# Performance work log

Hardware: AMD Instinct MI355X
Metric: run time of the kernel (lower is better)

Reference implementation:

```python
import jax, jax.numpy as jnp
import numpy as np

WINDOW = 60
DEPTH = 3
HIDDEN = 256
LN_EPS = 1e-5


def _lyndon_indices(d):
    # Lyndon words over alphabet {0..d-1}, lengths 2 and 3, lexicographic order
    # (signatory mode='words' extracts expanded-logsig coefficients at Lyndon words).
    i2 = np.array([(i, j) for i in range(d) for j in range(d) if (i, j) < (j, i)], dtype=np.int32)
    i3 = np.array([(i, j, k) for i in range(d) for j in range(d) for k in range(d)
                   if (i, j, k) < (j, k, i) and (i, j, k) < (k, i, j)], dtype=np.int32)
    return i2, i3


def _logsig_features(x):
    # x: [b, s, c] -> logsignature of time-augmented sliding windows: [b*s, sig_channels]
    b, s, c = x.shape
    d = c + 1
    # replicate-padded sliding windows via clipped gather (matches F.pad replicate + unfold)
    pos = jnp.clip(jnp.arange(s)[:, None] + jnp.arange(WINDOW)[None, :] - (WINDOW - 1), 0, s - 1)
    windows = x[:, pos, :]                                   # [b, s, W, c]
    t = jnp.linspace(0.0, 1.0, WINDOW, dtype=x.dtype)        # time augmentation channel
    t_b = jnp.broadcast_to(t[None, None, :, None], (b, s, WINDOW, 1))
    aug = jnp.concatenate([t_b, windows], axis=-1).reshape(b * s, WINDOW, d)
    N = b * s
    # basepoint=True: prepend zero point -> increments include the first point itself
    inc = jnp.diff(aug, axis=1, prepend=jnp.zeros((N, 1, d), aug.dtype))  # [N, W, d]
    inc_t = jnp.transpose(inc, (1, 0, 2))                    # [W, N, d]

    def chen_step(carry, v):
        S1, S2, S3 = carry
        vv = jnp.einsum('ni,nj->nij', v, v)
        vvv = jnp.einsum('nij,nk->nijk', vv, v)
        nS3 = S3 + jnp.einsum('nij,nk->nijk', S2, v) \
                 + 0.5 * jnp.einsum('ni,njk->nijk', S1, vv) + vvv / 6.0
        nS2 = S2 + jnp.einsum('ni,nj->nij', S1, v) + 0.5 * vv
        nS1 = S1 + v
        return (nS1, nS2, nS3), None

    init = (jnp.zeros((N, d), x.dtype), jnp.zeros((N, d, d), x.dtype), jnp.zeros((N, d, d, d), x.dtype))
    (S1, S2, S3), _ = jax.lax.scan(chen_step, init, inc_t)
    # log in truncated tensor algebra: log(1+x) = x - x^2/2 + x^3/3
    L1 = S1
    L2 = S2 - 0.5 * jnp.einsum('ni,nj->nij', S1, S1)
    L3 = (S3 - 0.5 * (jnp.einsum('ni,njk->nijk', S1, S2) + jnp.einsum('nij,nk->nijk', S2, S1))
          + jnp.einsum('ni,nj,nk->nijk', S1, S1, S1) / 3.0)
    i2, i3 = _lyndon_indices(d)
    f2 = L2[:, i2[:, 0], i2[:, 1]]
    f3 = L3[:, i3[:, 0], i3[:, 1], i3[:, 2]]
    return jnp.concatenate([L1, f2, f3], axis=-1)            # [N, sig_channels]


def setup_inputs() -> dict:
    key = jax.random.key(0)
    ks = jax.random.split(key, 5)
    b, s, c = 8, 2048, 8
    d = c + 1
    sig_channels = d + (d * d - d) // 2 + (d ** 3 - d) // 3  # 285 for d=9
    h2 = 2 * HIDDEN
    x = jax.random.normal(ks[0], (b, s, c), dtype=jnp.float32)
    w1 = jax.random.normal(ks[1], (sig_channels, h2), dtype=jnp.float32) / np.sqrt(sig_channels)
    b1 = jnp.zeros((h2,), jnp.float32)
    ln_g = jnp.ones((h2,), jnp.float32)
    ln_b = jnp.zeros((h2,), jnp.float32)
    w2 = jax.random.normal(ks[2], (h2, HIDDEN), dtype=jnp.float32) / np.sqrt(h2)
    b2 = jnp.zeros((HIDDEN,), jnp.float32)
    return {"x": x, "w1": w1, "b1": b1, "ln_g": ln_g, "ln_b": ln_b, "w2": w2, "b2": b2}


def reference(x, w1, b1, ln_g, ln_b, w2, b2):
    b, s, _ = x.shape
    feats = _logsig_features(x)                              # [b*s, sig_channels]
    h = jax.nn.gelu(feats @ w1 + b1, approximate=False)      # torch default GELU (erf)
    mu = jnp.mean(h, axis=-1, keepdims=True)
    var = jnp.var(h, axis=-1, keepdims=True)
    h = (h - mu) / jnp.sqrt(var + LN_EPS) * ln_g + ln_b      # LayerNorm; Dropout is eval no-op
    out = h @ w2 + b2
    return out.reshape(b, s, -1)
```

## Files before the change

kernel.cpp:

```cpp
#include <hip/hip_runtime.h>
#include <hip/hip_bf16.h>
#include <cstdint>
#include <cstddef>

typedef short short8 __attribute__((ext_vector_type(8)));
typedef float f32x4 __attribute__((ext_vector_type(4)));

#define NS    2048
#define KPAD  288
#define H2    512
#define HID   256
#define WPB   21
#define SBLK  98

__device__ __forceinline__ void gl2lds16(const void* g, void* l) {
    __builtin_amdgcn_global_load_lds(
        (const __attribute__((address_space(1))) void*)g,
        (__attribute__((address_space(3))) void*)l, 16, 0, 0);
}

__device__ __forceinline__ float geluf(float x) {
    return 0.5f * x * (1.0f + erff(x * 0.70710678118654752f));
}

__device__ __forceinline__ f32x4 shfl4(f32x4 v, int d) {
    f32x4 r;
    r[0] = __shfl_xor(v[0], d); r[1] = __shfl_xor(v[1], d);
    r[2] = __shfl_xor(v[2], d); r[3] = __shfl_xor(v[3], d);
    return r;
}

struct Tbl3 { short col[729]; };
static constexpr Tbl3 make_tbl3() {
    Tbl3 t{};
    for (int x = 0; x < 729; ++x) t.col[x] = -1;
    int r = 0;
    for (int i = 0; i < 9; ++i)
        for (int j = 0; j < 9; ++j)
            for (int k = 0; k < 9; ++k) {
                bool lt1 = (i < j) || (i == j && (j < k || (j == k && k < i)));
                bool lt2 = (i < k) || (i == k && (j < i || (j == i && k < j)));
                if (lt1 && lt2) { t.col[(i*9+j)*9+k] = (short)(45 + r); ++r; }
            }
    return t;
}
static constexpr Tbl3 TBL3 = make_tbl3();

#define SIG_STEP(RA,RB,RC) { \
    const float hh = 0.5f * S1i + vi * (1.0f / 6.0f); \
    { const float ra = S2ra + hh * v##RA; \
      S3a0 += ra*v0; S3a1 += ra*v1; S3a2 += ra*v2; S3a3 += ra*v3; S3a4 += ra*v4; \
      S3a5 += ra*v5; S3a6 += ra*v6; S3a7 += ra*v7; S3a8 += ra*v8; } \
    { const float rb = S2rb + hh * v##RB; \
      S3b0 += rb*v0; S3b1 += rb*v1; S3b2 += rb*v2; S3b3 += rb*v3; S3b4 += rb*v4; \
      S3b5 += rb*v5; S3b6 += rb*v6; S3b7 += rb*v7; S3b8 += rb*v8; } \
    { const float rc = S2rc + hh * v##RC; \
      S3c0 += rc*v0; S3c1 += rc*v1; S3c2 += rc*v2; S3c3 += rc*v3; S3c4 += rc*v4; \
      S3c5 += rc*v5; S3c6 += rc*v6; S3c7 += rc*v7; S3c8 += rc*v8; } \
    const float aa = S1i + 0.5f * vi; \
    S2ra += aa * v##RA; S2rb += aa * v##RB; S2rc += aa * v##RC; \
    S1i += vi; }

#define SIG_MAIN(RA,RB,RC) { \
     \
    const float* xr = &X[(g0 - lo) * 8]; \
    const float4 e0p = *(const float4*)xr; \
    const float4 e1p = *(const float4*)(xr + 4); \
    const float rabs = xr[ioff]; \
    { const float v0 = 0.f; \
      const float v1 = e0p.x, v2 = e0p.y, v3 = e0p.z, v4 = e0p.w; \
      const float v5 = e1p.x, v6 = e1p.y, v7 = e1p.z, v8 = e1p.w; \
      const float vi = (ci == 0) ? 0.f : rabs; \
      SIG_STEP(RA,RB,RC) } \
     \
    int gn = sm59 + 1; gn = (gn > 0) ? gn : 0; \
    const float* dp = &D[(gn - lo) * 8]; \
    float4 d0 = *(const float4*)dp; \
    float4 d1 = *(const float4*)(dp + 4); \
    float rn = dp[ioff]; \
    _Pragma("unroll 1") \
    for (int j = 1; j < 60; ++j) { \
      const float4 e0 = d0; const float4 e1 = d1; const float rs = rn; \
      int g2 = sm59 + j + 1; g2 = (g2 > 0) ? g2 : 0; \
      const float* dn = &D[(g2 - lo) * 8]; \
      d0 = *(const float4*)dn; d1 = *(const float4*)(dn + 4); rn = dn[ioff]; \
      const float v0 = DT; \
      const float v1 = e0.x, v2 = e0.y, v3 = e0.z, v4 = e0.w; \
      const float v5 = e1.x, v6 = e1.y, v7 = e1.z, v8 = e1.w; \
      const float vi = (ci == 0) ? DT : rs; \
      SIG_STEP(RA,RB,RC) \
    } }

#define SIG_ST(RA,RB,RC) \
    if (act) { \
        if ((RA) == 0) S1buf[widx * 9 + ci] = S1i; \
        float* sb = &S2buf[widx * 81 + ci * 9]; \
        sb[RA] = S2ra; sb[RB] = S2rb; sb[RC] = S2rc; \
    }

#define SIG_E2(SL,J2) if (ci < (J2)) { \
    const float val2 = S2r##SL - 0.5f * S1i * s1v##J2; \
    const int col2 = 9 + ci*8 - (ci*(ci-1))/2 + ((J2) - ci - 1); \
    frow[col2] = __float2bfloat16(val2); }

#define SIG_E3(SL,R,K) { const int col3 = TBL3.col[tb + (R)*9 + (K)]; \
    if (col3 >= 0) { \
        const float val3 = S3##SL##K \
            - 0.5f * (S1i * S2w[(R)*9+(K)] + S2r##SL * s1v##K) \
            + S1i * s1v##R * s1v##K * (1.0f/3.0f); \
        frow[col3] = __float2bfloat16(val3); } }

#define SIG_E3R(SL,R) SIG_E3(SL,R,0) SIG_E3(SL,R,1) SIG_E3(SL,R,2) SIG_E3(SL,R,3) \
    SIG_E3(SL,R,4) SIG_E3(SL,R,5) SIG_E3(SL,R,6) SIG_E3(SL,R,7) SIG_E3(SL,R,8)

#define SIG_EMIT(RA,RB,RC) \
    if (act) { \
        if ((RA) == 0) { \
            frow[ci] = __float2bfloat16(S1i); \
            if (ci == 0) { \
                const __hip_bfloat16 z16 = __float2bfloat16(0.0f); \
                frow[285] = z16; frow[286] = z16; frow[287] = z16; \
            } \
        } \
        SIG_E2(a,RA) SIG_E2(b,RB) SIG_E2(c,RC) \
        SIG_E3R(a,RA) SIG_E3R(b,RB) SIG_E3R(c,RC) \
    }

__global__ __launch_bounds__(576) __attribute__((amdgpu_waves_per_eu(1, 6)))
void sig_kernel(const float* __restrict__ x, __hip_bfloat16* __restrict__ feats) {
    __shared__ __align__(16) float X[82 * 8];
    __shared__ __align__(16) float D[82 * 8];
    __shared__ float S2buf[WPB * 81];
    __shared__ float S1buf[WPB * 9];

    const int blk = blockIdx.x;
    const int b   = blk / SBLK;
    const int s0  = (blk % SBLK) * WPB;
    const int lo  = (s0 - 59 > 0) ? (s0 - 59) : 0;
    const int hi  = (s0 + WPB - 1 < NS - 1) ? (s0 + WPB - 1) : (NS - 1);
    const int nrow = hi - lo + 1;
    const int tid = threadIdx.x;

    {
        const float4* src = (const float4*)(x + ((size_t)b * NS + lo) * 8);
        float4* dst = (float4*)X;
        const int n4 = nrow * 2;
        for (int t = tid; t < n4; t += 576) dst[t] = src[t];
    }
    __syncthreads();
    {
        const float4* X4 = (const float4*)X;
        float4* D4 = (float4*)D;
        for (int t = tid; t < 164; t += 576) {
            const int r = t >> 1;
            float4 dv = {0.f, 0.f, 0.f, 0.f};
            if (r > 0 && r < nrow) {
                const float4 a = X4[t], bb = X4[t - 2];
                dv.x = a.x - bb.x; dv.y = a.y - bb.y; dv.z = a.z - bb.z; dv.w = a.w - bb.w;
            }
            D4[t] = dv;
        }
    }
    __syncthreads();

    const int t3    = tid / 192;
    const int lt    = tid - t3 * 192;
    const int widx0 = lt / 9;
    const int ci    = lt - widx0 * 9;
    const int s_raw = s0 + widx0;
    const bool act  = (lt < 189) && (s_raw < NS);
    const int widx  = (widx0 < 20) ? widx0 : 20;
    int s = s0 + widx; if (s > NS - 1) s = NS - 1;

    float S3a0=0.f,S3a1=0.f,S3a2=0.f,S3a3=0.f,S3a4=0.f,S3a5=0.f,S3a6=0.f,S3a7=0.f,S3a8=0.f;
    float S3b0=0.f,S3b1=0.f,S3b2=0.f,S3b3=0.f,S3b4=0.f,S3b5=0.f,S3b6=0.f,S3b7=0.f,S3b8=0.f;
    float S3c0=0.f,S3c1=0.f,S3c2=0.f,S3c3=0.f,S3c4=0.f,S3c5=0.f,S3c6=0.f,S3c7=0.f,S3c8=0.f;
    float S2ra=0.f, S2rb=0.f, S2rc=0.f;
    float S1i = 0.f;
    const int ioff = (ci > 0) ? (ci - 1) : 0;
    const int sm59 = s - 59;
    const int g0   = (sm59 > 0) ? sm59 : 0;
    const float DT = 1.0f / 59.0f;

    if (t3 == 0)      { SIG_MAIN(0,1,2) }
    else if (t3 == 1) { SIG_MAIN(3,4,5) }
    else              { SIG_MAIN(6,7,8) }

    if (t3 == 0)      { SIG_ST(0,1,2) }
    else if (t3 == 1) { SIG_ST(3,4,5) }
    else              { SIG_ST(6,7,8) }
    __syncthreads();

    const float* s1p = &S1buf[widx * 9];
    const float s1v0=s1p[0], s1v1=s1p[1], s1v2=s1p[2], s1v3=s1p[3], s1v4=s1p[4];
    const float s1v5=s1p[5], s1v6=s1p[6], s1v7=s1p[7], s1v8=s1p[8];
    const float* S2w = &S2buf[widx * 81];
    const int tb = ci * 81;
    __hip_bfloat16* frow = feats + (size_t)(b * NS + s) * KPAD;

    if (t3 == 0)      { SIG_EMIT(0,1,2) }
    else if (t3 == 1) { SIG_EMIT(3,4,5) }
    else              { SIG_EMIT(6,7,8) }
}

__global__ void convert_w1(const float* __restrict__ w1, __hip_bfloat16* __restrict__ w1T) {
    const int n = blockIdx.x;
    const int k = threadIdx.x;
    const float v = (k < 285) ? w1[(size_t)k * H2 + n] : 0.0f;
    w1T[(size_t)n * KPAD + k] = __float2bfloat16(v);
}
__global__ void convert_w2(const float* __restrict__ w2, __hip_bfloat16* __restrict__ w2T) {
    const int n = blockIdx.x;
    const int k = threadIdx.x;
    w2T[(size_t)n * H2 + k] = __float2bfloat16(w2[(size_t)k * HID + n]);
}

#define G1_DECLACC(m) f32x4 acc##m##0 = {0.f,0.f,0.f,0.f}, acc##m##1 = {0.f,0.f,0.f,0.f}, \
                            acc##m##2 = {0.f,0.f,0.f,0.f}, acc##m##3 = {0.f,0.f,0.f,0.f};
#define G1_MFMA(m) { const short8 afr = *(const short8*)(ldsA + ((m)*16 + l16)*32 + quad*8); \
    acc##m##0 = __builtin_amdgcn_mfma_f32_16x16x32_bf16(afr, bfrag0, acc##m##0, 0,0,0); \
    acc##m##1 = __builtin_amdgcn_mfma_f32_16x16x32_bf16(afr, bfrag1, acc##m##1, 0,0,0); \
    acc##m##2 = __builtin_amdgcn_mfma_f32_16x16x32_bf16(afr, bfrag2, acc##m##2, 0,0,0); \
    acc##m##3 = __builtin_amdgcn_mfma_f32_16x16x32_bf16(afr, bfrag3, acc##m##3, 0,0,0); }
#define G1_GELU1(m,n) { \
    acc##m##n[0]=geluf(acc##m##n[0]+bias##n); acc##m##n[1]=geluf(acc##m##n[1]+bias##n); \
    acc##m##n[2]=geluf(acc##m##n[2]+bias##n); acc##m##n[3]=geluf(acc##m##n[3]+bias##n); }
#define G1_GELUR(m) G1_GELU1(m,0) G1_GELU1(m,1) G1_GELU1(m,2) G1_GELU1(m,3)
#define G1_LNS(m) f32x4 psum##m = acc##m##0 + acc##m##1 + acc##m##2 + acc##m##3; \
    f32x4 psq##m = acc##m##0*acc##m##0 + acc##m##1*acc##m##1 + acc##m##2*acc##m##2 + acc##m##3*acc##m##3;
#define G1_STP(m) { const int rrp = (m)*16 + quad*4; \
    lnpart[wave][rrp+0][0]=psum##m[0]; lnpart[wave][rrp+0][1]=psq##m[0]; \
    lnpart[wave][rrp+1][0]=psum##m[1]; lnpart[wave][rrp+1][1]=psq##m[1]; \
    lnpart[wave][rrp+2][0]=psum##m[2]; lnpart[wave][rrp+2][1]=psq##m[2]; \
    lnpart[wave][rrp+3][0]=psum##m[3]; lnpart[wave][rrp+3][1]=psq##m[3]; }
#define G1_LDST(m) f32x4 mu##m; f32x4 rstd##m; { const int rrl = (m)*16 + quad*4; \
    mu##m[0]=lnstat[rrl+0][0]; mu##m[1]=lnstat[rrl+1][0]; mu##m[2]=lnstat[rrl+2][0]; mu##m[3]=lnstat[rrl+3][0]; \
    rstd##m[0]=lnstat[rrl+0][1]; rstd##m[1]=lnstat[rrl+1][1]; rstd##m[2]=lnstat[rrl+2][1]; rstd##m[3]=lnstat[rrl+3][1]; }
#define G1_OUT(m,n) { const int colo = wave*64 + (n)*16 + l16; \
    f32x4 hv = (acc##m##n - mu##m) * rstd##m * gv##n + bv##n; \
    const int rro = (m)*16 + quad*4; \
    hbuf[(size_t)(m0+rro+0)*H2 + colo] = __float2bfloat16(hv[0]); \
    hbuf[(size_t)(m0+rro+1)*H2 + colo] = __float2bfloat16(hv[1]); \
    hbuf[(size_t)(m0+rro+2)*H2 + colo] = __float2bfloat16(hv[2]); \
    hbuf[(size_t)(m0+rro+3)*H2 + colo] = __float2bfloat16(hv[3]); }
#define G1_OUTR(m) G1_OUT(m,0) G1_OUT(m,1) G1_OUT(m,2) G1_OUT(m,3)

__global__ __launch_bounds__(512) __attribute__((amdgpu_waves_per_eu(1, 4)))
void gemm1_kernel(
        const __hip_bfloat16* __restrict__ feats,
        const __hip_bfloat16* __restrict__ w1T,
        const float* __restrict__ b1,
        const float* __restrict__ lng,
        const float* __restrict__ lnb,
        __hip_bfloat16* __restrict__ hbuf) {
    __shared__ __align__(16) __hip_bfloat16 ldsA[32 * 32];
    __shared__ __align__(16) __hip_bfloat16 ldsB[512 * 32];
    __shared__ float lnpart[8][32][2];
    __shared__ float lnstat[32][2];

    const int tid  = threadIdx.x;
    const int wave = tid >> 6;
    const int lane = tid & 63;
    const int quad = lane >> 4;
    const int l16  = lane & 15;
    const int m0   = blockIdx.x * 32;

    G1_DECLACC(0) G1_DECLACC(1)

#pragma unroll 1
    for (int kt = 0; kt < 9; ++kt) {
        const int K0 = kt * 32;
        if (tid < 128) {
            const int m = tid >> 2, kc = tid & 3;
            gl2lds16(feats + (size_t)(m0 + m) * KPAD + K0 + kc * 8,
                     (char*)ldsA + (tid & ~63) * 16);
        }
#pragma unroll
        for (int q = 0; q < 4; ++q) {
            const int chunk = q * 512 + tid;
            const int n = chunk >> 2, kc = chunk & 3;
            gl2lds16(w1T + (size_t)n * KPAD + K0 + kc * 8,
                     (char*)ldsB + (chunk & ~63) * 16);
        }
        __syncthreads();
        const __hip_bfloat16* bbase = ldsB + (wave * 64 + l16) * 32 + quad * 8;
        const short8 bfrag0 = *(const short8*)(bbase);
        const short8 bfrag1 = *(const short8*)(bbase + 16 * 32);
        const short8 bfrag2 = *(const short8*)(bbase + 32 * 32);
        const short8 bfrag3 = *(const short8*)(bbase + 48 * 32);
        G1_MFMA(0) G1_MFMA(1)
        __syncthreads();
    }

    const float bias0 = b1[wave*64 +  0 + l16];
    const float bias1 = b1[wave*64 + 16 + l16];
    const float bias2 = b1[wave*64 + 32 + l16];
    const float bias3 = b1[wave*64 + 48 + l16];
    G1_GELUR(0) G1_GELUR(1)

    G1_LNS(0) G1_LNS(1)
#pragma unroll
    for (int d = 1; d < 16; d <<= 1) {
        psum0 += shfl4(psum0, d); psq0 += shfl4(psq0, d);
        psum1 += shfl4(psum1, d); psq1 += shfl4(psq1, d);
    }
    if (l16 == 0) { G1_STP(0) G1_STP(1) }
    __syncthreads();
    if (tid < 32) {
        float su = 0.f, sq = 0.f;
#pragma unroll
        for (int w = 0; w < 8; ++w) { su += lnpart[w][tid][0]; sq += lnpart[w][tid][1]; }
        const float mu  = su * (1.0f / 512.0f);
        const float var = sq * (1.0f / 512.0f) - mu * mu;
        lnstat[tid][0] = mu;
        lnstat[tid][1] = rsqrtf(var + 1e-5f);
    }
    __syncthreads();
    const float gv0 = lng[wave*64 +  0 + l16], bv0 = lnb[wave*64 +  0 + l16];
    const float gv1 = lng[wave*64 + 16 + l16], bv1 = lnb[wave*64 + 16 + l16];
    const float gv2 = lng[wave*64 + 32 + l16], bv2 = lnb[wave*64 + 32 + l16];
    const float gv3 = lng[wave*64 + 48 + l16], bv3 = lnb[wave*64 + 48 + l16];
    G1_LDST(0) G1_LDST(1)
    G1_OUTR(0) G1_OUTR(1)
}

#define G2_DECL(m) f32x4 bcc##m##0 = {0.f,0.f,0.f,0.f}, bcc##m##1 = {0.f,0.f,0.f,0.f};
#define G2_MFMA(m) { const short8 afr = *(const short8*)(ldsA + ((m)*16 + l16)*32 + quad*8); \
    bcc##m##0 = __builtin_amdgcn_mfma_f32_16x16x32_bf16(afr, bfr0, bcc##m##0, 0,0,0); \
    bcc##m##1 = __builtin_amdgcn_mfma_f32_16x16x32_bf16(afr, bfr1, bcc##m##1, 0,0,0); }
#define G2_OUT(m) { const int rro = (m)*16 + quad*4; \
    out[(size_t)(m0+rro+0)*HID + c0i] = bcc##m##0[0] + bb0; \
    out[(size_t)(m0+rro+1)*HID + c0i] = bcc##m##0[1] + bb0; \
    out[(size_t)(m0+rro+2)*HID + c0i] = bcc##m##0[2] + bb0; \
    out[(size_t)(m0+rro+3)*HID + c0i] = bcc##m##0[3] + bb0; \
    out[(size_t)(m0+rro+0)*HID + c1i] = bcc##m##1[0] + bb1; \
    out[(size_t)(m0+rro+1)*HID + c1i] = bcc##m##1[1] + bb1; \
    out[(size_t)(m0+rro+2)*HID + c1i] = bcc##m##1[2] + bb1; \
    out[(size_t)(m0+rro+3)*HID + c1i] = bcc##m##1[3] + bb1; }

__global__ __launch_bounds__(512) __attribute__((amdgpu_waves_per_eu(1, 4)))
void gemm2_kernel(
        const __hip_bfloat16* __restrict__ hbuf,
        const __hip_bfloat16* __restrict__ w2T,
        const float* __restrict__ b2,
        float* __restrict__ out) {
    __shared__ __align__(16) __hip_bfloat16 ldsA[32 * 32];
    __shared__ __align__(16) __hip_bfloat16 ldsB[256 * 32];
    const int tid  = threadIdx.x;
    const int wave = tid >> 6;
    const int lane = tid & 63;
    const int quad = lane >> 4;
    const int l16  = lane & 15;
    const int m0   = blockIdx.x * 32;

    G2_DECL(0) G2_DECL(1)

#pragma unroll 1
    for (int kt = 0; kt < 16; ++kt) {
        const int K0 = kt * 32;
        if (tid < 128) {
            const int m = tid >> 2, kc = tid & 3;
            gl2lds16(hbuf + (size_t)(m0 + m) * H2 + K0 + kc * 8,
                     (char*)ldsA + (tid & ~63) * 16);
        }
#pragma unroll
        for (int q = 0; q < 2; ++q) {
            const int chunk = q * 512 + tid;
            const int n = chunk >> 2, kc = chunk & 3;
            gl2lds16(w2T + (size_t)n * H2 + K0 + kc * 8,
                     (char*)ldsB + (chunk & ~63) * 16);
        }
        __syncthreads();
        const __hip_bfloat16* bbase = ldsB + (wave * 32 + l16) * 32 + quad * 8;
        const short8 bfr0 = *(const short8*)(bbase);
        const short8 bfr1 = *(const short8*)(bbase + 16 * 32);
        G2_MFMA(0) G2_MFMA(1)
        __syncthreads();
    }
    const float bb0 = b2[wave*32 +  0 + l16];
    const float bb1 = b2[wave*32 + 16 + l16];
    const int c0i = wave*32 +  0 + l16;
    const int c1i = wave*32 + 16 + l16;
    G2_OUT(0) G2_OUT(1)
}

extern "C" void kernel_launch(void* const* d_in, const int* in_sizes, int n_in,
                              void* d_out, int out_size, void* d_ws, size_t ws_size,
                              hipStream_t stream) {
    const float* x   = (const float*)d_in[0];
    const float* w1  = (const float*)d_in[1];
    const float* b1  = (const float*)d_in[2];
    const float* lng = (const float*)d_in[3];
    const float* lnb = (const float*)d_in[4];
    const float* w2  = (const float*)d_in[5];
    const float* b2  = (const float*)d_in[6];
    float* out = (float*)d_out;

    char* ws = (char*)d_ws;
    __hip_bfloat16* feats = (__hip_bfloat16*)(ws);
    __hip_bfloat16* hbuf  = (__hip_bfloat16*)(ws + 9437184);
    __hip_bfloat16* w1T   = (__hip_bfloat16*)(ws + 9437184 + 16777216);
    __hip_bfloat16* w2T   = (__hip_bfloat16*)(ws + 9437184 + 16777216 + 294912);

    convert_w1<<<dim3(512), dim3(288), 0, stream>>>(w1, w1T);
    convert_w2<<<dim3(256), dim3(512), 0, stream>>>(w2, w2T);
    sig_kernel<<<dim3(8 * SBLK), dim3(576), 0, stream>>>(x, feats);
    gemm1_kernel<<<dim3(16384 / 32), dim3(512), 0, stream>>>(feats, w1T, b1, lng, lnb, hbuf);
    gemm2_kernel<<<dim3(16384 / 32), dim3(512), 0, stream>>>(hbuf, w2T, b2, out);
}
```

Baseline: 171.8 us.

## Retile GEMMs to 128x128, fold LayerNorm into GEMM2 epilogue, reshape sig kernel

Both GEMMs now use 128x128 tiles per 256-thread block instead of 32-row strips that reload the whole weight matrix for every block. LayerNorm is no longer applied in GEMM1: row sums and sums of squares are accumulated with atomics, and the gamma, beta and bias terms are folded into a pre-scaled W2 plus per-column vectors, so GEMM2 applies the normalization algebraically in its epilogue. The signature kernel moves to smaller blocks of 7 windows with a pre-padded increment buffer that removes per-step clamping, and uses packed float2 FMAs. In exchange the GELU output is stored un-normalized in bf16, the variance is computed as E[x^2]-mu^2, and an extra memset plus atomic traffic are added.

```diff
diff --git a/kernel.cpp b/kernel.cpp
--- a/kernel.cpp
+++ b/kernel.cpp
@@ -5,24 +5,25 @@
 
 typedef short short8 __attribute__((ext_vector_type(8)));
 typedef float f32x4 __attribute__((ext_vector_type(4)));
+typedef float f32x2 __attribute__((ext_vector_type(2)));
 
 #define NS    2048
 #define KPAD  288
 #define H2    512
 #define HID   256
-#define WPB   21
-#define SBLK  98
+#define WPB   7
+#define SBLK  293
+
+#define MFMA(a,b,c) __builtin_amdgcn_mfma_f32_16x16x32_bf16((a),(b),(c),0,0,0)
 
 __device__ __forceinline__ void gl2lds16(const void* g, void* l) {
     __builtin_amdgcn_global_load_lds(
         (const __attribute__((address_space(1))) void*)g,
         (__attribute__((address_space(3))) void*)l, 16, 0, 0);
 }
-
 __device__ __forceinline__ float geluf(float x) {
     return 0.5f * x * (1.0f + erff(x * 0.70710678118654752f));
 }
-
 __device__ __forceinline__ f32x4 shfl4(f32x4 v, int d) {
     f32x4 r;
     r[0] = __shfl_xor(v[0], d); r[1] = __shfl_xor(v[1], d);
@@ -46,49 +47,41 @@
 }
 static constexpr Tbl3 TBL3 = make_tbl3();
 
-#define SIG_STEP(RA,RB,RC) { \
-    const float hh = 0.5f * S1i + vi * (1.0f / 6.0f); \
-    { const float ra = S2ra + hh * v##RA; \
-      S3a0 += ra*v0; S3a1 += ra*v1; S3a2 += ra*v2; S3a3 += ra*v3; S3a4 += ra*v4; \
-      S3a5 += ra*v5; S3a6 += ra*v6; S3a7 += ra*v7; S3a8 += ra*v8; } \
-    { const float rb = S2rb + hh * v##RB; \
-      S3b0 += rb*v0; S3b1 += rb*v1; S3b2 += rb*v2; S3b3 += rb*v3; S3b4 += rb*v4; \
-      S3b5 += rb*v5; S3b6 += rb*v6; S3b7 += rb*v7; S3b8 += rb*v8; } \
-    { const float rc = S2rc + hh * v##RC; \
-      S3c0 += rc*v0; S3c1 += rc*v1; S3c2 += rc*v2; S3c3 += rc*v3; S3c4 += rc*v4; \
-      S3c5 += rc*v5; S3c6 += rc*v6; S3c7 += rc*v7; S3c8 += rc*v8; } \
+#define SIG_STEP(VA_,VB_,VC_) { \
+    const float hh = 0.5f * S1i + vi * (1.0f/6.0f); \
+    const float ra = S2ra + hh * (VA_); \
+    const float rb = S2rb + hh * (VB_); \
+    const float rc = S2rc + hh * (VC_); \
+    const f32x2 ra2 = {ra, ra}, rb2 = {rb, rb}, rc2 = {rc, rc}; \
+    S3sa += ra * v0; S3pa0 += ra2*vp0; S3pa1 += ra2*vp1; S3pa2 += ra2*vp2; S3pa3 += ra2*vp3; \
+    S3sb += rb * v0; S3pb0 += rb2*vp0; S3pb1 += rb2*vp1; S3pb2 += rb2*vp2; S3pb3 += rb2*vp3; \
+    S3sc += rc * v0; S3pc0 += rc2*vp0; S3pc1 += rc2*vp1; S3pc2 += rc2*vp2; S3pc3 += rc2*vp3; \
     const float aa = S1i + 0.5f * vi; \
-    S2ra += aa * v##RA; S2rb += aa * v##RB; S2rc += aa * v##RC; \
+    S2ra += aa * (VA_); S2rb += aa * (VB_); S2rc += aa * (VC_); \
     S1i += vi; }
 
-#define SIG_MAIN(RA,RB,RC) { \
-     \
-    const float* xr = &X[(g0 - lo) * 8]; \
-    const float4 e0p = *(const float4*)xr; \
-    const float4 e1p = *(const float4*)(xr + 4); \
-    const float rabs = xr[ioff]; \
-    { const float v0 = 0.f; \
-      const float v1 = e0p.x, v2 = e0p.y, v3 = e0p.z, v4 = e0p.w; \
-      const float v5 = e1p.x, v6 = e1p.y, v7 = e1p.z, v8 = e1p.w; \
-      const float vi = (ci == 0) ? 0.f : rabs; \
-      SIG_STEP(RA,RB,RC) } \
-     \
-    int gn = sm59 + 1; gn = (gn > 0) ? gn : 0; \
-    const float* dp = &D[(gn - lo) * 8]; \
-    float4 d0 = *(const float4*)dp; \
-    float4 d1 = *(const float4*)(dp + 4); \
-    float rn = dp[ioff]; \
-    _Pragma("unroll 1") \
+#define SIG_MAIN(VA_,VB_,VC_) { \
+    { const float* xr = &X[(g0 - lo) * 8]; \
+      const float4 e0 = *(const float4*)xr; \
+      const float4 e1 = *(const float4*)(xr + 4); \
+      const float rs = xr[ioff]; \
+      const float v0 = 0.0f; \
+      const f32x2 vp0 = {e0.x, e0.y}, vp1 = {e0.z, e0.w}, vp2 = {e1.x, e1.y}, vp3 = {e1.z, e1.w}; \
+      const float vi = (ci == 0) ? 0.0f : rs; \
+      SIG_STEP(VA_,VB_,VC_) } \
+    const float* pd = &PD[(sm59 + 1 - lo + 59) * 8]; \
+    float4 d0 = *(const float4*)pd; \
+    float4 d1 = *(const float4*)(pd + 4); \
+    float rn = pd[ioff]; \
+    _Pragma("unroll 2") \
     for (int j = 1; j < 60; ++j) { \
       const float4 e0 = d0; const float4 e1 = d1; const float rs = rn; \
-      int g2 = sm59 + j + 1; g2 = (g2 > 0) ? g2 : 0; \
-      const float* dn = &D[(g2 - lo) * 8]; \
-      d0 = *(const float4*)dn; d1 = *(const float4*)(dn + 4); rn = dn[ioff]; \
+      pd += 8; \
+      d0 = *(const float4*)pd; d1 = *(const float4*)(pd + 4); rn = pd[ioff]; \
       const float v0 = DT; \
-      const float v1 = e0.x, v2 = e0.y, v3 = e0.z, v4 = e0.w; \
-      const float v5 = e1.x, v6 = e1.y, v7 = e1.z, v8 = e1.w; \
+      const f32x2 vp0 = {e0.x, e0.y}, vp1 = {e0.z, e0.w}, vp2 = {e1.x, e1.y}, vp3 = {e1.z, e1.w}; \
       const float vi = (ci == 0) ? DT : rs; \
-      SIG_STEP(RA,RB,RC) \
+      SIG_STEP(VA_,VB_,VC_) \
     } }
 
 #define SIG_ST(RA,RB,RC) \
@@ -98,6 +91,16 @@
         sb[RA] = S2ra; sb[RB] = S2rb; sb[RC] = S2rc; \
     }
 
+#define S3EL0(SL) S3s##SL
+#define S3EL1(SL) S3p##SL##0[0]
+#define S3EL2(SL) S3p##SL##0[1]
+#define S3EL3(SL) S3p##SL##1[0]
+#define S3EL4(SL) S3p##SL##1[1]
+#define S3EL5(SL) S3p##SL##2[0]
+#define S3EL6(SL) S3p##SL##2[1]
+#define S3EL7(SL) S3p##SL##3[0]
+#define S3EL8(SL) S3p##SL##3[1]
+
 #define SIG_E2(SL,J2) if (ci < (J2)) { \
     const float val2 = S2r##SL - 0.5f * S1i * s1v##J2; \
     const int col2 = 9 + ci*8 - (ci*(ci-1))/2 + ((J2) - ci - 1); \
@@ -105,7 +108,7 @@
 
 #define SIG_E3(SL,R,K) { const int col3 = TBL3.col[tb + (R)*9 + (K)]; \
     if (col3 >= 0) { \
-        const float val3 = S3##SL##K \
+        const float val3 = S3EL##K(SL) \
             - 0.5f * (S1i * S2w[(R)*9+(K)] + S2r##SL * s1v##K) \
             + S1i * s1v##R * s1v##K * (1.0f/3.0f); \
         frow[col3] = __float2bfloat16(val3); } }
@@ -126,10 +129,10 @@
         SIG_E3R(a,RA) SIG_E3R(b,RB) SIG_E3R(c,RC) \
     }
 
-__global__ __launch_bounds__(576) __attribute__((amdgpu_waves_per_eu(1, 6)))
+__global__ __launch_bounds__(192) __attribute__((amdgpu_waves_per_eu(1, 6)))
 void sig_kernel(const float* __restrict__ x, __hip_bfloat16* __restrict__ feats) {
-    __shared__ __align__(16) float X[82 * 8];
-    __shared__ __align__(16) float D[82 * 8];
+    __shared__ __align__(16) float X[66 * 8];
+    __shared__ __align__(16) float PD[126 * 8];
     __shared__ float S2buf[WPB * 81];
     __shared__ float S1buf[WPB * 9];
 
@@ -143,38 +146,39 @@
 
     {
         const float4* src = (const float4*)(x + ((size_t)b * NS + lo) * 8);
-        float4* dst = (float4*)X;
+        float4* X4 = (float4*)X;
         const int n4 = nrow * 2;
-        for (int t = tid; t < n4; t += 576) dst[t] = src[t];
+        for (int t = tid; t < n4; t += 192) X4[t] = src[t];
     }
     __syncthreads();
     {
         const float4* X4 = (const float4*)X;
-        float4* D4 = (float4*)D;
-        for (int t = tid; t < 164; t += 576) {
-            const int r = t >> 1;
+        float4* PD4 = (float4*)PD;
+        for (int t = tid; t < 252; t += 192) {
+            const int p = t >> 1;
+            const int r = p - 59;
             float4 dv = {0.f, 0.f, 0.f, 0.f};
             if (r > 0 && r < nrow) {
-                const float4 a = X4[t], bb = X4[t - 2];
+                const float4 a = X4[t - 118], bb = X4[t - 120];
                 dv.x = a.x - bb.x; dv.y = a.y - bb.y; dv.z = a.z - bb.z; dv.w = a.w - bb.w;
             }
-            D4[t] = dv;
+            PD4[t] = dv;
         }
     }
     __syncthreads();
 
-    const int t3    = tid / 192;
-    const int lt    = tid - t3 * 192;
+    const int t3    = tid >> 6;
+    const int lt    = tid & 63;
     const int widx0 = lt / 9;
     const int ci    = lt - widx0 * 9;
-    const int s_raw = s0 + widx0;
-    const bool act  = (lt < 189) && (s_raw < NS);
-    const int widx  = (widx0 < 20) ? widx0 : 20;
+    const bool act  = (lt < 63) && (s0 + widx0 < NS);
+    const int widx  = (widx0 < WPB - 1) ? widx0 : WPB - 1;
     int s = s0 + widx; if (s > NS - 1) s = NS - 1;
 
-    float S3a0=0.f,S3a1=0.f,S3a2=0.f,S3a3=0.f,S3a4=0.f,S3a5=0.f,S3a6=0.f,S3a7=0.f,S3a8=0.f;
-    float S3b0=0.f,S3b1=0.f,S3b2=0.f,S3b3=0.f,S3b4=0.f,S3b5=0.f,S3b6=0.f,S3b7=0.f,S3b8=0.f;
-    float S3c0=0.f,S3c1=0.f,S3c2=0.f,S3c3=0.f,S3c4=0.f,S3c5=0.f,S3c6=0.f,S3c7=0.f,S3c8=0.f;
+    float S3sa=0.f, S3sb=0.f, S3sc=0.f;
+    f32x2 S3pa0={0.f,0.f},S3pa1={0.f,0.f},S3pa2={0.f,0.f},S3pa3={0.f,0.f};
+    f32x2 S3pb0={0.f,0.f},S3pb1={0.f,0.f},S3pb2={0.f,0.f},S3pb3={0.f,0.f};
+    f32x2 S3pc0={0.f,0.f},S3pc1={0.f,0.f},S3pc2={0.f,0.f},S3pc3={0.f,0.f};
     float S2ra=0.f, S2rb=0.f, S2rc=0.f;
     float S1i = 0.f;
     const int ioff = (ci > 0) ? (ci - 1) : 0;
@@ -182,9 +186,9 @@
     const int g0   = (sm59 > 0) ? sm59 : 0;
     const float DT = 1.0f / 59.0f;
 
-    if (t3 == 0)      { SIG_MAIN(0,1,2) }
-    else if (t3 == 1) { SIG_MAIN(3,4,5) }
-    else              { SIG_MAIN(6,7,8) }
+    if (t3 == 0)      { SIG_MAIN(v0,   e0.x, e0.y) }
+    else if (t3 == 1) { SIG_MAIN(e0.z, e0.w, e1.x) }
+    else              { SIG_MAIN(e1.y, e1.z, e1.w) }
 
     if (t3 == 0)      { SIG_ST(0,1,2) }
     else if (t3 == 1) { SIG_ST(3,4,5) }
@@ -209,179 +213,149 @@
     const float v = (k < 285) ? w1[(size_t)k * H2 + n] : 0.0f;
     w1T[(size_t)n * KPAD + k] = __float2bfloat16(v);
 }
-__global__ void convert_w2(const float* __restrict__ w2, __hip_bfloat16* __restrict__ w2T) {
-    const int n = blockIdx.x;
-    const int k = threadIdx.x;
-    w2T[(size_t)n * H2 + k] = __float2bfloat16(w2[(size_t)k * HID + n]);
-}
-
-#define G1_DECLACC(m) f32x4 acc##m##0 = {0.f,0.f,0.f,0.f}, acc##m##1 = {0.f,0.f,0.f,0.f}, \
-                            acc##m##2 = {0.f,0.f,0.f,0.f}, acc##m##3 = {0.f,0.f,0.f,0.f};
-#define G1_MFMA(m) { const short8 afr = *(const short8*)(ldsA + ((m)*16 + l16)*32 + quad*8); \
-    acc##m##0 = __builtin_amdgcn_mfma_f32_16x16x32_bf16(afr, bfrag0, acc##m##0, 0,0,0); \
-    acc##m##1 = __builtin_amdgcn_mfma_f32_16x16x32_bf16(afr, bfrag1, acc##m##1, 0,0,0); \
-    acc##m##2 = __builtin_amdgcn_mfma_f32_16x16x32_bf16(afr, bfrag2, acc##m##2, 0,0,0); \
-    acc##m##3 = __builtin_amdgcn_mfma_f32_16x16x32_bf16(afr, bfrag3, acc##m##3, 0,0,0); }
-#define G1_GELU1(m,n) { \
-    acc##m##n[0]=geluf(acc##m##n[0]+bias##n); acc##m##n[1]=geluf(acc##m##n[1]+bias##n); \
-    acc##m##n[2]=geluf(acc##m##n[2]+bias##n); acc##m##n[3]=geluf(acc##m##n[3]+bias##n); }
-#define G1_GELUR(m) G1_GELU1(m,0) G1_GELU1(m,1) G1_GELU1(m,2) G1_GELU1(m,3)
-#define G1_LNS(m) f32x4 psum##m = acc##m##0 + acc##m##1 + acc##m##2 + acc##m##3; \
-    f32x4 psq##m = acc##m##0*acc##m##0 + acc##m##1*acc##m##1 + acc##m##2*acc##m##2 + acc##m##3*acc##m##3;
-#define G1_STP(m) { const int rrp = (m)*16 + quad*4; \
-    lnpart[wave][rrp+0][0]=psum##m[0]; lnpart[wave][rrp+0][1]=psq##m[0]; \
-    lnpart[wave][rrp+1][0]=psum##m[1]; lnpart[wave][rrp+1][1]=psq##m[1]; \
-    lnpart[wave][rrp+2][0]=psum##m[2]; lnpart[wave][rrp+2][1]=psq##m[2]; \
-    lnpart[wave][rrp+3][0]=psum##m[3]; lnpart[wave][rrp+3][1]=psq##m[3]; }
-#define G1_LDST(m) f32x4 mu##m; f32x4 rstd##m; { const int rrl = (m)*16 + quad*4; \
-    mu##m[0]=lnstat[rrl+0][0]; mu##m[1]=lnstat[rrl+1][0]; mu##m[2]=lnstat[rrl+2][0]; mu##m[3]=lnstat[rrl+3][0]; \
-    rstd##m[0]=lnstat[rrl+0][1]; rstd##m[1]=lnstat[rrl+1][1]; rstd##m[2]=lnstat[rrl+2][1]; rstd##m[3]=lnstat[rrl+3][1]; }
-#define G1_OUT(m,n) { const int colo = wave*64 + (n)*16 + l16; \
-    f32x4 hv = (acc##m##n - mu##m) * rstd##m * gv##n + bv##n; \
-    const int rro = (m)*16 + quad*4; \
-    hbuf[(size_t)(m0+rro+0)*H2 + colo] = __float2bfloat16(hv[0]); \
-    hbuf[(size_t)(m0+rro+1)*H2 + colo] = __float2bfloat16(hv[1]); \
-    hbuf[(size_t)(m0+rro+2)*H2 + colo] = __float2bfloat16(hv[2]); \
-    hbuf[(size_t)(m0+rro+3)*H2 + colo] = __float2bfloat16(hv[3]); }
-#define G1_OUTR(m) G1_OUT(m,0) G1_OUT(m,1) G1_OUT(m,2) G1_OUT(m,3)
-
-__global__ __launch_bounds__(512) __attribute__((amdgpu_waves_per_eu(1, 4)))
-void gemm1_kernel(
-        const __hip_bfloat16* __restrict__ feats,
-        const __hip_bfloat16* __restrict__ w1T,
-        const float* __restrict__ b1,
-        const float* __restrict__ lng,
-        const float* __restrict__ lnb,
-        __hip_bfloat16* __restrict__ hbuf) {
-    __shared__ __align__(16) __hip_bfloat16 ldsA[32 * 32];
-    __shared__ __align__(16) __hip_bfloat16 ldsB[512 * 32];
-    __shared__ float lnpart[8][32][2];
-    __shared__ float lnstat[32][2];
-
+__global__ void convert_w2g(const float* __restrict__ w2, const float* __restrict__ lng,
+                            const float* __restrict__ lnb, const float* __restrict__ b2,
+                            __hip_bfloat16* __restrict__ w2g, float* __restrict__ gw,
+                            float* __restrict__ cvec) {
+    const int n = blockIdx.x, k = threadIdx.x;
+    const float wv = w2[(size_t)k * HID + n];
+    const float a = lng[k] * wv;
+    const float c = lnb[k] * wv;
+    w2g[(size_t)n * H2 + k] = __float2bfloat16(a);
+    float ra = a, rc = c;
+#pragma unroll
+    for (int d = 1; d < 64; d <<= 1) { ra += __shfl_xor(ra, d); rc += __shfl_xor(rc, d); }
+    __shared__ float r1[8], r2[8];
+    const int wv_ = k >> 6, ln = k & 63;
+    if (ln == 0) { r1[wv_] = ra; r2[wv_] = rc; }
+    __syncthreads();
+    if (k == 0) {
+        float sa = 0.f, sc = 0.f;
+#pragma unroll
+        for (int i = 0; i < 8; ++i) { sa += r1[i]; sc += r2[i]; }
+        gw[n] = sa; cvec[n] = sc + b2[n];
+    }
+}
+
+#define GDECL \
+    f32x4 acc00={0,0,0,0},acc01={0,0,0,0},acc02={0,0,0,0},acc03={0,0,0,0}; \
+    f32x4 acc10={0,0,0,0},acc11={0,0,0,0},acc12={0,0,0,0},acc13={0,0,0,0}; \
+    f32x4 acc20={0,0,0,0},acc21={0,0,0,0},acc22={0,0,0,0},acc23={0,0,0,0}; \
+    f32x4 acc30={0,0,0,0},acc31={0,0,0,0},acc32={0,0,0,0},acc33={0,0,0,0};
+
+#define GMROW(mf) { const short8 av = *(const short8*)(abase + (mf)*512); \
+    acc##mf##0 = MFMA(av, b0v, acc##mf##0); acc##mf##1 = MFMA(av, b1v, acc##mf##1); \
+    acc##mf##2 = MFMA(av, b2v, acc##mf##2); acc##mf##3 = MFMA(av, b3v, acc##mf##3); }
+
+#define GEMM_KLOOP(APTR, BPTR, KD, KSTEPS) \
+    _Pragma("unroll 1") \
+    for (int kt = 0; kt < (KSTEPS); ++kt) { \
+        const int K0 = kt * 32; \
+        { int c = tid; \
+          gl2lds16((APTR) + (size_t)(m0 + (c>>2))*(KD) + K0 + (c&3)*8, (char*)ldsA + (c & ~63)*16); \
+          gl2lds16((BPTR) + (size_t)(n0 + (c>>2))*(KD) + K0 + (c&3)*8, (char*)ldsB + (c & ~63)*16); \
+          c = tid + 256; \
+          gl2lds16((APTR) + (size_t)(m0 + (c>>2))*(KD) + K0 + (c&3)*8, (char*)ldsA + (c & ~63)*16); \
+          gl2lds16((BPTR) + (size_t)(n0 + (c>>2))*(KD) + K0 + (c&3)*8, (char*)ldsB + (c & ~63)*16); } \
+        __syncthreads(); \
+        const __hip_bfloat16* abase = ldsA + (mh + l16)*32 + quad*8; \
+        const __hip_bfloat16* bbase = ldsB + (nh + l16)*32 + quad*8; \
+        const short8 b0v = *(const short8*)(bbase); \
+        const short8 b1v = *(const short8*)(bbase + 512); \
+        const short8 b2v = *(const short8*)(bbase + 1024); \
+        const short8 b3v = *(const short8*)(bbase + 1536); \
+        GMROW(0) GMROW(1) GMROW(2) GMROW(3) \
+        __syncthreads(); \
+    }
+
+#define G1EP(mf,nf) { \
+    const int colv = n0 + nh + (nf)*16 + l16; \
+    const float bv = bias[colv]; \
+    f32x4 e; \
+    e[0] = geluf(acc##mf##nf[0] + bv); e[1] = geluf(acc##mf##nf[1] + bv); \
+    e[2] = geluf(acc##mf##nf[2] + bv); e[3] = geluf(acc##mf##nf[3] + bv); \
+    const int rrow = m0 + mh + (mf)*16 + quad*4; \
+    h1[(size_t)(rrow+0)*H2 + colv] = __float2bfloat16(e[0]); \
+    h1[(size_t)(rrow+1)*H2 + colv] = __float2bfloat16(e[1]); \
+    h1[(size_t)(rrow+2)*H2 + colv] = __float2bfloat16(e[2]); \
+    h1[(size_t)(rrow+3)*H2 + colv] = __float2bfloat16(e[3]); \
+    sum##mf += e; sq##mf += e*e; }
+
+#define G1RED(mf) { \
+    f32x4 s = sum##mf, q = sq##mf; \
+    s += shfl4(s,1); q += shfl4(q,1); s += shfl4(s,2); q += shfl4(q,2); \
+    s += shfl4(s,4); q += shfl4(q,4); s += shfl4(s,8); q += shfl4(q,8); \
+    if (l16 == 0) { const int rrow = m0 + mh + (mf)*16 + quad*4; \
+        atomicAdd(&stats[2*(rrow+0)],   s[0]); atomicAdd(&stats[2*(rrow+0)+1], q[0]); \
+        atomicAdd(&stats[2*(rrow+1)],   s[1]); atomicAdd(&stats[2*(rrow+1)+1], q[1]); \
+        atomicAdd(&stats[2*(rrow+2)],   s[2]); atomicAdd(&stats[2*(rrow+2)+1], q[2]); \
+        atomicAdd(&stats[2*(rrow+3)],   s[3]); atomicAdd(&stats[2*(rrow+3)+1], q[3]); } }
+
+__global__ __launch_bounds__(256) __attribute__((amdgpu_waves_per_eu(1, 4)))
+void gemm1_kernel(const __hip_bfloat16* __restrict__ feats,
+                  const __hip_bfloat16* __restrict__ w1T,
+                  const float* __restrict__ bias,
+                  __hip_bfloat16* __restrict__ h1,
+                  float* __restrict__ stats) {
+    __shared__ __align__(16) __hip_bfloat16 ldsA[128 * 32];
+    __shared__ __align__(16) __hip_bfloat16 ldsB[128 * 32];
     const int tid  = threadIdx.x;
     const int wave = tid >> 6;
     const int lane = tid & 63;
     const int quad = lane >> 4;
     const int l16  = lane & 15;
-    const int m0   = blockIdx.x * 32;
-
-    G1_DECLACC(0) G1_DECLACC(1)
-
-#pragma unroll 1
-    for (int kt = 0; kt < 9; ++kt) {
-        const int K0 = kt * 32;
-        if (tid < 128) {
-            const int m = tid >> 2, kc = tid & 3;
-            gl2lds16(feats + (size_t)(m0 + m) * KPAD + K0 + kc * 8,
-                     (char*)ldsA + (tid & ~63) * 16);
-        }
-#pragma unroll
-        for (int q = 0; q < 4; ++q) {
-            const int chunk = q * 512 + tid;
-            const int n = chunk >> 2, kc = chunk & 3;
-            gl2lds16(w1T + (size_t)n * KPAD + K0 + kc * 8,
-                     (char*)ldsB + (chunk & ~63) * 16);
-        }
-        __syncthreads();
-        const __hip_bfloat16* bbase = ldsB + (wave * 64 + l16) * 32 + quad * 8;
-        const short8 bfrag0 = *(const short8*)(bbase);
-        const short8 bfrag1 = *(const short8*)(bbase + 16 * 32);
-        const short8 bfrag2 = *(const short8*)(bbase + 32 * 32);
-        const short8 bfrag3 = *(const short8*)(bbase + 48 * 32);
-        G1_MFMA(0) G1_MFMA(1)
-        __syncthreads();
-    }
-
-    const float bias0 = b1[wave*64 +  0 + l16];
-    const float bias1 = b1[wave*64 + 16 + l16];
-    const float bias2 = b1[wave*64 + 32 + l16];
-    const float bias3 = b1[wave*64 + 48 + l16];
-    G1_GELUR(0) G1_GELUR(1)
-
-    G1_LNS(0) G1_LNS(1)
-#pragma unroll
-    for (int d = 1; d < 16; d <<= 1) {
-        psum0 += shfl4(psum0, d); psq0 += shfl4(psq0, d);
-        psum1 += shfl4(psum1, d); psq1 += shfl4(psq1, d);
-    }
-    if (l16 == 0) { G1_STP(0) G1_STP(1) }
-    __syncthreads();
-    if (tid < 32) {
-        float su = 0.f, sq = 0.f;
-#pragma unroll
-        for (int w = 0; w < 8; ++w) { su += lnpart[w][tid][0]; sq += lnpart[w][tid][1]; }
-        const float mu  = su * (1.0f / 512.0f);
-        const float var = sq * (1.0f / 512.0f) - mu * mu;
-        lnstat[tid][0] = mu;
-        lnstat[tid][1] = rsqrtf(var + 1e-5f);
-    }
-    __syncthreads();
-    const float gv0 = lng[wave*64 +  0 + l16], bv0 = lnb[wave*64 +  0 + l16];
-    const float gv1 = lng[wave*64 + 16 + l16], bv1 = lnb[wave*64 + 16 + l16];
-    const float gv2 = lng[wave*64 + 32 + l16], bv2 = lnb[wave*64 + 32 + l16];
-    const float gv3 = lng[wave*64 + 48 + l16], bv3 = lnb[wave*64 + 48 + l16];
-    G1_LDST(0) G1_LDST(1)
-    G1_OUTR(0) G1_OUTR(1)
-}
-
-#define G2_DECL(m) f32x4 bcc##m##0 = {0.f,0.f,0.f,0.f}, bcc##m##1 = {0.f,0.f,0.f,0.f};
-#define G2_MFMA(m) { const short8 afr = *(const short8*)(ldsA + ((m)*16 + l16)*32 + quad*8); \
-    bcc##m##0 = __builtin_amdgcn_mfma_f32_16x16x32_bf16(afr, bfr0, bcc##m##0, 0,0,0); \
-    bcc##m##1 = __builtin_amdgcn_mfma_f32_16x16x32_bf16(afr, bfr1, bcc##m##1, 0,0,0); }
-#define G2_OUT(m) { const int rro = (m)*16 + quad*4; \
-    out[(size_t)(m0+rro+0)*HID + c0i] = bcc##m##0[0] + bb0; \
-    out[(size_t)(m0+rro+1)*HID + c0i] = bcc##m##0[1] + bb0; \
-    out[(size_t)(m0+rro+2)*HID + c0i] = bcc##m##0[2] + bb0; \
-    out[(size_t)(m0+rro+3)*HID + c0i] = bcc##m##0[3] + bb0; \
-    out[(size_t)(m0+rro+0)*HID + c1i] = bcc##m##1[0] + bb1; \
-    out[(size_t)(m0+rro+1)*HID + c1i] = bcc##m##1[1] + bb1; \
-    out[(size_t)(m0+rro+2)*HID + c1i] = bcc##m##1[2] + bb1; \
-    out[(size_t)(m0+rro+3)*HID + c1i] = bcc##m##1[3] + bb1; }
-
-__global__ __launch_bounds__(512) __attribute__((amdgpu_waves_per_eu(1, 4)))
-void gemm2_kernel(
-        const __hip_bfloat16* __restrict__ hbuf,
-        const __hip_bfloat16* __restrict__ w2T,
-        const float* __restrict__ b2,
-        float* __restrict__ out) {
-    __shared__ __align__(16) __hip_bfloat16 ldsA[32 * 32];
-    __shared__ __align__(16) __hip_bfloat16 ldsB[256 * 32];
+    const int mh   = (wave >> 1) * 64;
+    const int nh   = (wave & 1) * 64;
+    const int m0   = blockIdx.x * 128;
+    const int n0   = blockIdx.y * 128;
+    GDECL
+    GEMM_KLOOP(feats, w1T, KPAD, 9)
+    f32x4 sum0={0,0,0,0},sum1={0,0,0,0},sum2={0,0,0,0},sum3={0,0,0,0};
+    f32x4 sq0={0,0,0,0},sq1={0,0,0,0},sq2={0,0,0,0},sq3={0,0,0,0};
+    G1EP(0,0) G1EP(0,1) G1EP(0,2) G1EP(0,3)
+    G1EP(1,0) G1EP(1,1) G1EP(1,2) G1EP(1,3)
+    G1EP(2,0) G1EP(2,1) G1EP(2,2) G1EP(2,3)
+    G1EP(3,0) G1EP(3,1) G1EP(3,2) G1EP(3,3)
+    G1RED(0) G1RED(1) G1RED(2) G1RED(3)
+}
+
+#define STATR(r) { const float su = stats[2*(rrow+(r))]; const float qu = stats[2*(rrow+(r))+1]; \
+    const float m_ = su * (1.0f/512.0f); const float v_ = qu * (1.0f/512.0f) - m_*m_; \
+    muv[r] = m_; rsv[r] = rsqrtf(v_ + 1e-5f); }
+
+#define G2C(mf,nf) { const int colv = n0 + nh + (nf)*16 + l16; \
+    const float g_ = gw[colv], c_ = cvec[colv]; \
+    out[(size_t)(rrow+0)*HID + colv] = rsv[0]*(acc##mf##nf[0] - muv[0]*g_) + c_; \
+    out[(size_t)(rrow+1)*HID + colv] = rsv[1]*(acc##mf##nf[1] - muv[1]*g_) + c_; \
+    out[(size_t)(rrow+2)*HID + colv] = rsv[2]*(acc##mf##nf[2] - muv[2]*g_) + c_; \
+    out[(size_t)(rrow+3)*HID + colv] = rsv[3]*(acc##mf##nf[3] - muv[3]*g_) + c_; }
+
+#define G2EP(mf) { const int rrow = m0 + mh + (mf)*16 + quad*4; \
+    f32x4 muv, rsv; \
+    STATR(0) STATR(1) STATR(2) STATR(3) \
+    G2C(mf,0) G2C(mf,1) G2C(mf,2) G2C(mf,3) }
+
+__global__ __launch_bounds__(256) __attribute__((amdgpu_waves_per_eu(1, 4)))
+void gemm2_kernel(const __hip_bfloat16* __restrict__ h1,
+                  const __hip_bfloat16* __restrict__ w2g,
+                  const float* __restrict__ stats,
+                  const float* __restrict__ gw,
+                  const float* __restrict__ cvec,
+                  float* __restrict__ out) {
+    __shared__ __align__(16) __hip_bfloat16 ldsA[128 * 32];
+    __shared__ __align__(16) __hip_bfloat16 ldsB[128 * 32];
     const int tid  = threadIdx.x;
     const int wave = tid >> 6;
     const int lane = tid & 63;
     const int quad = lane >> 4;
     const int l16  = lane & 15;
-    const int m0   = blockIdx.x * 32;
-
-    G2_DECL(0) G2_DECL(1)
-
-#pragma unroll 1
-    for (int kt = 0; kt < 16; ++kt) {
-        const int K0 = kt * 32;
-        if (tid < 128) {
-            const int m = tid >> 2, kc = tid & 3;
-            gl2lds16(hbuf + (size_t)(m0 + m) * H2 + K0 + kc * 8,
-                     (char*)ldsA + (tid & ~63) * 16);
-        }
-#pragma unroll
-        for (int q = 0; q < 2; ++q) {
-            const int chunk = q * 512 + tid;
-            const int n = chunk >> 2, kc = chunk & 3;
-            gl2lds16(w2T + (size_t)n * H2 + K0 + kc * 8,
-                     (char*)ldsB + (chunk & ~63) * 16);
-        }
-        __syncthreads();
-        const __hip_bfloat16* bbase = ldsB + (wave * 32 + l16) * 32 + quad * 8;
-        const short8 bfr0 = *(const short8*)(bbase);
-        const short8 bfr1 = *(const short8*)(bbase + 16 * 32);
-        G2_MFMA(0) G2_MFMA(1)
-        __syncthreads();
-    }
-    const float bb0 = b2[wave*32 +  0 + l16];
-    const float bb1 = b2[wave*32 + 16 + l16];
-    const int c0i = wave*32 +  0 + l16;
-    const int c1i = wave*32 + 16 + l16;
-    G2_OUT(0) G2_OUT(1)
+    const int mh   = (wave >> 1) * 64;
+    const int nh   = (wave & 1) * 64;
+    const int m0   = blockIdx.x * 128;
+    const int n0   = blockIdx.y * 128;
+    GDECL
+    GEMM_KLOOP(h1, w2g, H2, 16)
+    G2EP(0) G2EP(1) G2EP(2) G2EP(3)
 }
 
 extern "C" void kernel_launch(void* const* d_in, const int* in_sizes, int n_in,
@@ -398,13 +372,17 @@
 
     char* ws = (char*)d_ws;
     __hip_bfloat16* feats = (__hip_bfloat16*)(ws);
-    __hip_bfloat16* hbuf  = (__hip_bfloat16*)(ws + 9437184);
-    __hip_bfloat16* w1T   = (__hip_bfloat16*)(ws + 9437184 + 16777216);
-    __hip_bfloat16* w2T   = (__hip_bfloat16*)(ws + 9437184 + 16777216 + 294912);
-
+    __hip_bfloat16* h1    = (__hip_bfloat16*)(ws + 9437184);
+    __hip_bfloat16* w1T   = (__hip_bfloat16*)(ws + 26214400);
+    __hip_bfloat16* w2g   = (__hip_bfloat16*)(ws + 26509312);
+    float*          gw    = (float*)(ws + 26771456);
+    float*          cvec  = (float*)(ws + 26775552);
+    float*          stats = (float*)(ws + 26779648);
+
+    hipMemsetAsync(stats, 0, 16384 * 2 * sizeof(float), stream);
     convert_w1<<<dim3(512), dim3(288), 0, stream>>>(w1, w1T);
-    convert_w2<<<dim3(256), dim3(512), 0, stream>>>(w2, w2T);
-    sig_kernel<<<dim3(8 * SBLK), dim3(576), 0, stream>>>(x, feats);
-    gemm1_kernel<<<dim3(16384 / 32), dim3(512), 0, stream>>>(feats, w1T, b1, lng, lnb, hbuf);
-    gemm2_kernel<<<dim3(16384 / 32), dim3(512), 0, stream>>>(hbuf, w2T, b2, out);
-}
+    convert_w2g<<<dim3(256), dim3(512), 0, stream>>>(w2, lng, lnb, b2, w2g, gw, cvec);
+    sig_kernel<<<dim3(8 * SBLK), dim3(192), 0, stream>>>(x, feats);
+    gemm1_kernel<<<dim3(128, 4), dim3(256), 0, stream>>>(feats, w1T, b1, h1, stats);
+    gemm2_kernel<<<dim3(128, 2), dim3(256), 0, stream>>>(h1, w2g, stats, gw, cvec, out);
+}
```

Result: faster. 163.7 us (-4.7%).
